# Optimization experiments

Hardware: AMD Instinct MI355X
Metric: run time of the kernel (lower is better)

The kernel has to match this reference:

```python
import jax, jax.numpy as jnp
import numpy as np
import math

B, L, D = 2, 4096, 1024
H, DK, DV = 4, 256, 256
CHUNK = 32
PROB_FLOOR = 0.02


def _l2norm(x, eps=1e-6):
    return x * jax.lax.rsqrt(jnp.sum(x * x, -1, keepdims=True) + eps)


def _silu(x):
    return x * jax.nn.sigmoid(x)


def _short_conv(x, w):
    # x: (b, l, c); w: (c, K). Depthwise causal conv + SiLU (ShortConvolution).
    K = w.shape[-1]
    xp = jnp.pad(x, ((0, 0), (K - 1, 0), (0, 0)))
    y = sum(xp[:, j:j + x.shape[1], :] * w[:, j] for j in range(K))
    return _silu(y)


def _fir_conv(x, filt):
    # x: (b, l, h, d); filt: (h, d, K). Depthwise causal FIR, no activation.
    b, l, h, d = x.shape
    K = filt.shape[-1]
    xf = jnp.pad(x.reshape(b, l, h * d).transpose(0, 2, 1), ((0, 0), (0, 0), (K - 1, 0)))
    w = filt.reshape(h * d, 1, K)
    y = jax.lax.conv_general_dilated(xf, w, (1,), 'VALID',
                                     dimension_numbers=('NCH', 'OIH', 'NCH'),
                                     feature_group_count=h * d)
    return y.transpose(0, 2, 1).reshape(b, l, h, d)


def _delta_rule_chunkwise(q, k, v, beta, chunk=CHUNK):
    # q,k: (b,h,L,dk); v: (b,h,L,dv); beta: (b,h,L). L % chunk == 0.
    b, h, Lq, dk = q.shape
    dv = v.shape[-1]
    n = Lq // chunk
    q = _l2norm(q)
    k = _l2norm(k)
    v = v * beta[..., None]
    kb = k * beta[..., None]
    rs = lambda t: t.reshape(b, h, n, chunk, t.shape[-1])
    qc, kc, vc, kbc = rs(q), rs(k), rs(v), rs(kb)
    strict_lower = jnp.tril(jnp.ones((chunk, chunk), bool), -1)
    # M = strictly-lower part of k_beta @ k^T; the in-place row recursion in the
    # torch code computes (I + M)^{-1} (unit lower-triangular inverse).
    M = jnp.where(strict_lower, jnp.einsum('bhncd,bhnmd->bhncm', kbc, kc), 0.0)
    eye = jnp.eye(chunk, dtype=q.dtype)
    T = jax.scipy.linalg.solve_triangular(eye + M, jnp.broadcast_to(eye, M.shape),
                                          lower=True, unit_diagonal=True)
    u = T @ vc       # (b,h,n,c,dv)
    w = T @ kbc      # (b,h,n,c,dk)
    incl_lower = jnp.tril(jnp.ones((chunk, chunk), bool), 0)

    def step(S, xs):
        q_i, k_i, u_i, w_i = xs  # (b,h,c,d)
        attn = jnp.where(incl_lower, q_i @ k_i.swapaxes(-1, -2), 0.0)
        u_adj = u_i - w_i @ S
        out_i = q_i @ S + attn @ u_adj
        S = S + k_i.swapaxes(-1, -2) @ u_adj
        return S, out_i

    S0 = jnp.zeros((b, h, dk, dv), q.dtype)
    xs = tuple(jnp.moveaxis(t, 2, 0) for t in (qc, kc, u, w))
    S, out = jax.lax.scan(step, S0, xs)
    out = jnp.moveaxis(out, 0, 2).reshape(b, h, Lq, dv)
    return out, S


def _rmsnorm(x, w, eps=1e-5):
    return x * jax.lax.rsqrt(jnp.mean(x * x, -1, keepdims=True) + eps) * w


def _per_head_stats(x):
    mean = jnp.mean(x, -1, keepdims=True)
    var = jnp.var(x, -1, keepdims=True)
    am = jnp.mean(jnp.abs(x), -1, keepdims=True)
    l2 = jnp.sqrt(jnp.sum(x * x, -1, keepdims=True))
    return jnp.concatenate([mean, var, am, l2], -1)  # (...,4)


def setup_inputs() -> dict:
    key = jax.random.key(0)
    ks = jax.random.split(key, 16)
    s = 0.02
    hidden_gate = D * 2 // 2  # fusion_hidden_mult=2 -> 1024
    gate_in_dim = D + 16
    inp = {
        'hidden_states': jax.random.normal(ks[0], (B, L, D), jnp.float32),
        'q_w': jax.random.normal(ks[1], (D, D), jnp.float32) * s,
        'k_w': jax.random.normal(ks[2], (D, D), jnp.float32) * s,
        'v_w': jax.random.normal(ks[3], (D, D), jnp.float32) * s,
        'b_w': jax.random.normal(ks[4], (H, D), jnp.float32) * s,
        'q_cw': jax.random.normal(ks[5], (D, 4), jnp.float32) * s,
        'k_cw': jax.random.normal(ks[6], (D, 4), jnp.float32) * s,
        'v_cw': jax.random.normal(ks[7], (D, 4), jnp.float32) * s,
        'fir_short_w': jax.random.normal(ks[8], (H, DV, 5), jnp.float32) * s,
        'fir_long_w': jax.random.normal(ks[9], (H, DV, 64), jnp.float32) * s,
        'mlp1_w': jax.random.normal(ks[10], (hidden_gate, gate_in_dim), jnp.float32) * s,
        'mlp1_b': jnp.zeros((hidden_gate,), jnp.float32),
        'mlp2_w': jax.random.normal(ks[11], (4, hidden_gate), jnp.float32) * s,
        'mlp2_b': jnp.array([-0.5, -0.5, 1.0, 3.0], jnp.float32),
        'logit_temp': jnp.full((1,), math.log(math.expm1(0.7)), jnp.float32),
        'conv_res_logit': jnp.full((H,), -2.0, jnp.float32),
        'norm_w': jnp.ones((DV,), jnp.float32),
        'o_w': jax.random.normal(ks[12], (D, D), jnp.float32) * s,
    }
    return inp


def _forward(hidden_states, q_w, k_w, v_w, b_w, q_cw, k_cw, v_cw,
             fir_short_w, fir_long_w, mlp1_w, mlp1_b, mlp2_w, mlp2_b,
             logit_temp, conv_res_logit, norm_w, o_w):
    b, l, _ = hidden_states.shape
    # projections + short causal depthwise convs (SiLU, qk_activation='silu')
    q_in = _short_conv(hidden_states @ q_w.T, q_cw)
    k_in = _short_conv(hidden_states @ k_w.T, k_cw)
    v_in = _short_conv(hidden_states @ v_w.T, v_cw)
    q = q_in.reshape(b, l, H, DK)
    k = k_in.reshape(b, l, H, DK)
    v_direct = v_in.reshape(b, l, H, DV)
    # qk_activation='silu' handled in conv; qk_norm='l2' handled inside delta rule
    beta = jnp.maximum(jax.nn.sigmoid(hidden_states @ b_w.T), 1e-6)  # (b,l,H)
    delta_out, _S = _delta_rule_chunkwise(
        q.transpose(0, 2, 1, 3), k.transpose(0, 2, 1, 3),
        v_direct.transpose(0, 2, 1, 3), beta.transpose(0, 2, 1))
    delta_out = delta_out.transpose(0, 2, 1, 3)  # (b,l,H,DV)
    local_short = _fir_conv(v_direct, fir_short_w)
    local_long = _fir_conv(v_direct, fir_long_w)
    stats = jnp.concatenate([_per_head_stats(local_short), _per_head_stats(local_long),
                             _per_head_stats(delta_out), _per_head_stats(v_direct)], -1)  # (b,l,H,16)
    hs_exp = jnp.broadcast_to(hidden_states[:, :, None, :], (b, l, H, hidden_states.shape[-1]))
    gate_in = jnp.concatenate([hs_exp, stats], -1)  # (b,l,H,D+16)
    h1 = jax.nn.gelu(gate_in @ mlp1_w.T + mlp1_b)
    logits = h1 @ mlp2_w.T + mlp2_b  # (b,l,H,4)
    temp = jax.nn.softplus(logit_temp)
    p = jax.nn.softmax(logits / temp, -1)
    p = jnp.maximum(p, PROB_FLOOR)
    p = p / jnp.sum(p, -1, keepdims=True)
    o = (p[..., 0:1] * local_short + p[..., 1:2] * local_long +
         p[..., 2:3] * delta_out + p[..., 3:4] * v_direct)
    # balanced residual conv injection (per-head learned static gate)
    o = o + jax.nn.sigmoid(conv_res_logit)[None, None, :, None] * local_short
    o = _rmsnorm(o, norm_w)
    o = o.reshape(b, l, H * DV) @ o_w.T
    return o


def reference(hidden_states, q_w, k_w, v_w, b_w, q_cw, k_cw, v_cw,
              fir_short_w, fir_long_w, mlp1_w, mlp1_b, mlp2_w, mlp2_b,
              logit_temp, conv_res_logit, norm_w, o_w):
    return _forward(hidden_states, q_w, k_w, v_w, b_w, q_cw, k_cw, v_cw,
                    fir_short_w, fir_long_w, mlp1_w, mlp1_b, mlp2_w, mlp2_b,
                    logit_temp, conv_res_logit, norm_w, o_w)
```

## Files before the change

kernel.cpp:

```cpp
#include <hip/hip_runtime.h>
#include <hip/hip_bf16.h>
#include <math.h>

#define NB 2
#define NL 4096
#define ND 1024
#define NH 4
#define NDK 256
#define NDV 256
#define NCH 128
#define NBL (NB*NL)

typedef __attribute__((ext_vector_type(8))) short short8;
typedef __attribute__((ext_vector_type(4))) short short4v;
typedef __attribute__((ext_vector_type(4))) float float4v;

#define MFMA16(a,b,c) __builtin_amdgcn_mfma_f32_16x16x32_bf16(a,b,c,0,0,0)

__device__ __forceinline__ short f2bs(float f){
  union { __hip_bfloat16 h; short s; } u; u.h = __float2bfloat16(f); return u.s;
}
__device__ __forceinline__ float bs2f(short s){
  union { float f; unsigned u; } u; u.u = ((unsigned)(unsigned short)s) << 16; return u.f;
}
__device__ __forceinline__ void store_c(float* p, float v){ *p = v; }
__device__ __forceinline__ void store_c(short* p, float v){ *p = f2bs(v); }

__device__ __forceinline__ void gload16(const short* g, short* l){
  __builtin_amdgcn_global_load_lds(
      (const __attribute__((address_space(1))) unsigned int*)g,
      (__attribute__((address_space(3))) unsigned int*)l, 16, 0, 0);
}
__device__ __forceinline__ void lds_barrier(){
  asm volatile("s_waitcnt lgkmcnt(0)" ::: "memory");
  __builtin_amdgcn_s_barrier();
  asm volatile("" ::: "memory");
}

__global__ void k_cast8(const float* __restrict__ s, short* __restrict__ d, int n8){
  int i = blockIdx.x*256 + threadIdx.x;
  if(i >= n8) return;
  const float4v a = *(const float4v*)(s + (size_t)i*8);
  const float4v b = *(const float4v*)(s + (size_t)i*8 + 4);
  short8 o;
  #pragma unroll
  for(int j=0;j<4;j++){ o[j] = f2bs(a[j]); o[4+j] = f2bs(b[j]); }
  *(short8*)(d + (size_t)i*8) = o;
}
__global__ void k_cast_w1a(const float* __restrict__ s, short* __restrict__ d){
  int i = blockIdx.x*256 + threadIdx.x;
  int r = i >> 7, c0 = (i & 127)*8;
  const float* sp = s + (size_t)r*1040 + c0;
  const float4v a = *(const float4v*)sp;
  const float4v b = *(const float4v*)(sp + 4);
  short8 o;
  #pragma unroll
  for(int j=0;j<4;j++){ o[j] = f2bs(a[j]); o[4+j] = f2bs(b[j]); }
  *(short8*)(d + (size_t)r*1024 + c0) = o;
}

template<typename OT>
__launch_bounds__(256)
__global__ void k_gemm(const short* __restrict__ A, const short* __restrict__ Bt,
                       OT* __restrict__ C, int M, int N, int K){
  __shared__ short As[128*32];
  __shared__ short Bs[128*32];
  const int tid = threadIdx.x;
  const int w = tid >> 6, lane = tid & 63, lr = lane & 15, lg = lane >> 4;
  const int bm = blockIdx.x*128 + (w >> 1)*64;
  const int bn = blockIdx.y*128 + (w & 1)*64;
  float4v acc[4][4];
  #pragma unroll
  for(int i=0;i<4;i++)
    #pragma unroll
    for(int j=0;j<4;j++) acc[i][j] = (float4v){0.f,0.f,0.f,0.f};
  const short* ga0 = A  + (size_t)(blockIdx.x*128 + (tid>>2))*K + (tid&3)*8;
  const short* ga1 = ga0 + (size_t)64*K;
  const short* gb0 = Bt + (size_t)(blockIdx.y*128 + (tid>>2))*K + (tid&3)*8;
  const short* gb1 = gb0 + (size_t)64*K;
  short* la0 = As + w*512;
  short* la1 = As + 2048 + w*512;
  short* lb0 = Bs + w*512;
  short* lb1 = Bs + 2048 + w*512;
  const int arow = (w>>1)*64, brow = (w&1)*64;
  for(int kk=0; kk<K; kk+=32){
    gload16(ga0+kk, la0);
    gload16(ga1+kk, la1);
    gload16(gb0+kk, lb0);
    gload16(gb1+kk, lb1);
    __syncthreads();
    short8 a[4], b[4];
    #pragma unroll
    for(int i=0;i<4;i++) a[i] = *(const short8*)(As + (arow + i*16 + lr)*32 + lg*8);
    #pragma unroll
    for(int j=0;j<4;j++) b[j] = *(const short8*)(Bs + (brow + j*16 + lr)*32 + lg*8);
    #pragma unroll
    for(int i=0;i<4;i++)
      #pragma unroll
      for(int j=0;j<4;j++)
        acc[i][j] = MFMA16(a[i], b[j], acc[i][j]);
    __syncthreads();
  }
  #pragma unroll
  for(int i=0;i<4;i++){
    int row0 = bm + i*16 + lg*4;
    #pragma unroll
    for(int j=0;j<4;j++){
      OT* cp = C + (size_t)row0*N + bn + j*16 + lr;
      #pragma unroll
      for(int r=0;r<4;r++) store_c(cp + (size_t)r*N, acc[i][j][r]);
    }
  }
}

__global__ void k_conv_silu(const short* __restrict__ x, const float* __restrict__ wgt,
                            short* __restrict__ y){
  int i8 = blockIdx.x*256 + threadIdx.x;
  int c0 = (i8 & 127)*8;
  int l = (i8 >> 7) & (NL-1);
  size_t base = (size_t)i8*8;
  short8 xv[4];
  #pragma unroll
  for(int t=0;t<4;t++)
    xv[t] = (l >= t) ? *(const short8*)(x + base - (size_t)t*1024)
                     : (short8){0,0,0,0,0,0,0,0};
  short8 o;
  #pragma unroll
  for(int j=0;j<8;j++){
    const float4v w4 = *(const float4v*)(wgt + (c0+j)*4);
    float acc = 0.f;
    #pragma unroll
    for(int t=0;t<4;t++) if(l >= t) acc += bs2f(xv[t][j]) * w4[3-t];
    o[j] = f2bs(acc / (1.f + __expf(-acc)));
  }
  *(short8*)(y + base) = o;
}

__global__ void k_beta(const float* __restrict__ hs, const float* __restrict__ bw,
                       float* __restrict__ beta){
  int w = threadIdx.x >> 6, lane = threadIdx.x & 63;
  int bl = blockIdx.x*4 + w;
  const float* x = hs + (size_t)bl*1024;
  float a[4] = {0.f,0.f,0.f,0.f};
  for(int d=lane; d<1024; d+=64){
    float xv = x[d];
    #pragma unroll
    for(int hh=0;hh<4;hh++) a[hh] += xv * bw[hh*1024 + d];
  }
  #pragma unroll
  for(int off=32; off; off>>=1)
    #pragma unroll
    for(int hh=0;hh<4;hh++) a[hh] += __shfl_down(a[hh], off);
  if(lane == 0)
    #pragma unroll
    for(int hh=0;hh<4;hh++)
      beta[(size_t)bl*4 + hh] = fmaxf(1.f/(1.f+__expf(-a[hh])), 1e-6f);
}

#define PADA 260
__launch_bounds__(256)
__global__ void k_phaseA(const short* __restrict__ q, const short* __restrict__ k,
                         const short* __restrict__ v, const float* __restrict__ beta,
                         short* __restrict__ qn_o, short* __restrict__ wn_o,
                         short* __restrict__ kT_o, short* __restrict__ at_o,
                         float* __restrict__ u_o){
  __shared__ float qn[32*PADA];
  __shared__ float kn[32*PADA];
  __shared__ float vb[32*PADA];
  __shared__ float kb[32*PADA];
  __shared__ float Ml[32*33];
  __shared__ float bet[32];
  const int tid = threadIdx.x;
  const int n = blockIdx.x % NCH;
  const int h = (blockIdx.x / NCH) % NH;
  const int b = blockIdx.x / (NCH*NH);
  size_t rowbase = ((size_t)b*NL + n*32)*1024 + h*256;
  if(tid < 32) bet[tid] = beta[((size_t)b*NL + n*32 + tid)*4 + h];
  for(int r=0;r<32;r++){
    qn[r*PADA + tid] = bs2f(q[rowbase + (size_t)r*1024 + tid]);
    kn[r*PADA + tid] = bs2f(k[rowbase + (size_t)r*1024 + tid]);
    vb[r*PADA + tid] = bs2f(v[rowbase + (size_t)r*1024 + tid]);
  }
  __syncthreads();
  {
    int row = tid >> 3, sub = tid & 7;
    float sq = 0.f, sk = 0.f;
    for(int kk=0; kk<32; kk++){
      int d = sub + 8*kk;
      float a0 = qn[row*PADA+d]; sq += a0*a0;
      float a1 = kn[row*PADA+d]; sk += a1*a1;
    }
    #pragma unroll
    for(int off=1; off<8; off<<=1){ sq += __shfl_xor(sq, off); sk += __shfl_xor(sk, off); }
    float rq = rsqrtf(sq + 1e-6f), rk = rsqrtf(sk + 1e-6f);
    float be = bet[row];
    for(int kk=0; kk<32; kk++){
      int d = sub + 8*kk;
      qn[row*PADA+d] *= rq;
      float kv = kn[row*PADA+d]*rk;
      kn[row*PADA+d] = kv;
      kb[row*PADA+d] = kv*be;
      vb[row*PADA+d] *= be;
    }
  }
  __syncthreads();
  {
    int w = tid >> 6, lane = tid & 63, lr = lane & 15, lg = lane >> 4;
    int m0 = (w & 1)*16;
    const float* Asrc = (w < 2) ? kb : qn;
    float4v acc0 = (float4v){0.f,0.f,0.f,0.f}, acc1 = (float4v){0.f,0.f,0.f,0.f};
    for(int kc=0; kc<8; kc++){
      int kof = kc*32 + lg*8;
      short8 af, b0, b1;
      const float* ap  = Asrc + (m0+lr)*PADA + kof;
      const float* bp0 = kn + lr*PADA + kof;
      const float* bp1 = kn + (16+lr)*PADA + kof;
      #pragma unroll
      for(int j=0;j<8;j++){ af[j]=f2bs(ap[j]); b0[j]=f2bs(bp0[j]); b1[j]=f2bs(bp1[j]); }
      acc0 = MFMA16(af, b0, acc0);
      acc1 = MFMA16(af, b1, acc1);
    }
    if(w < 2){
      #pragma unroll
      for(int r=0;r<4;r++){
        int row = m0 + lg*4 + r;
        Ml[row*33 + lr]      = (lr      < row) ? acc0[r] : 0.f;
        Ml[row*33 + 16 + lr] = ((16+lr) < row) ? acc1[r] : 0.f;
      }
    } else {
      size_t abase = (size_t)blockIdx.x * 1024;
      #pragma unroll
      for(int r=0;r<4;r++){
        int row = m0 + lg*4 + r;
        at_o[abase + row*32 + lr]      = (lr      <= row) ? f2bs(acc0[r]) : (short)0;
        at_o[abase + row*32 + 16 + lr] = ((16+lr) <= row) ? f2bs(acc1[r]) : (short)0;
      }
    }
  }
  __syncthreads();
  {
    int d = tid;
    for(int i=1;i<32;i++){
      float su = 0.f, sw = 0.f;
      const float* Mr = Ml + i*33;
      for(int t=0;t<i;t++){
        float m = Mr[t];
        su += m * vb[t*PADA + d];
        sw += m * kb[t*PADA + d];
      }
      vb[i*PADA + d] -= su;
      kb[i*PADA + d] -= sw;
    }
  }
  __syncthreads();
  {
    size_t obase = (size_t)blockIdx.x * 8192;
    for(int it=0; it<32; it++){
      int idx = it*256 + tid;
      qn_o[obase + idx] = f2bs(qn[it*PADA + tid]);
      wn_o[obase + idx] = f2bs(-kb[it*PADA + tid]);
      u_o [obase + idx] = vb[it*PADA + tid];
      int tt = idx & 31, dd = idx >> 5;
      kT_o[obase + idx] = f2bs(kn[tt*PADA + dd]);
    }
  }
}

struct FragsB {
  short8 a[8];
  short8 kt[4];
  short8 at;
  float4v u;
};

__device__ __forceinline__ void loadFrags(FragsB& f, size_t cb,
    const short* __restrict__ qn, const short* __restrict__ wn,
    const short* __restrict__ kT, const short* __restrict__ at,
    const float* __restrict__ u, int w, int lr, int lg, int m0, int c0){
  const short* kT_b = kT + cb*8192;
  #pragma unroll
  for(int mi=0;mi<4;mi++)
    f.kt[mi] = *(const short8*)(kT_b + ((w*4+mi)*16 + lr)*32 + lg*8);
  if(w < 2){
    const short* wn_b = wn + cb*8192;
    #pragma unroll
    for(int kc=0;kc<8;kc++)
      f.a[kc] = *(const short8*)(wn_b + (m0+lr)*256 + kc*32 + lg*8);
    const float* up = u + cb*8192 + (size_t)(m0 + lg*4)*256 + c0 + lr;
    #pragma unroll
    for(int r=0;r<4;r++) f.u[r] = up[(size_t)r*256];
  } else {
    const short* qn_b = qn + cb*8192;
    #pragma unroll
    for(int kc=0;kc<8;kc++)
      f.a[kc] = *(const short8*)(qn_b + (m0+lr)*256 + kc*32 + lg*8);
    f.at = *(const short8*)(at + cb*1024 + (m0+lr)*32 + lg*8);
  }
}

__device__ __forceinline__ void computeChunk(const FragsB& f, int n,
    float4v (&Sreg)[4], float* __restrict__ ua, short* __restrict__ ScT,
    short* __restrict__ dout, int b, int h, int c0,
    int w, int lr, int lg, int m0, int swz){
  char* scb = (char*)ScT;
  lds_barrier();
  float4v oacc = (float4v){0.f,0.f,0.f,0.f};
  if(w < 2){
    float4v acc = f.u, acc2 = (float4v){0.f,0.f,0.f,0.f};
    #pragma unroll
    for(int kc=0;kc<4;kc++){
      short8 s0 = *(const short8*)(scb + (((lr<<9) + ((kc*32 + lg*8)<<1)) ^ swz));
      short8 s1 = *(const short8*)(scb + (((lr<<9) + (((kc+4)*32 + lg*8)<<1)) ^ swz));
      acc  = MFMA16(f.a[kc],   s0, acc);
      acc2 = MFMA16(f.a[kc+4], s1, acc2);
    }
    #pragma unroll
    for(int r=0;r<4;r++) ua[(m0 + lg*4 + r)*18 + lr] = acc[r] + acc2[r];
  } else {
    float4v acc2 = (float4v){0.f,0.f,0.f,0.f};
    #pragma unroll
    for(int kc=0;kc<4;kc++){
      short8 s0 = *(const short8*)(scb + (((lr<<9) + ((kc*32 + lg*8)<<1)) ^ swz));
      short8 s1 = *(const short8*)(scb + (((lr<<9) + (((kc+4)*32 + lg*8)<<1)) ^ swz));
      oacc = MFMA16(f.a[kc],   s0, oacc);
      acc2 = MFMA16(f.a[kc+4], s1, acc2);
    }
    #pragma unroll
    for(int r=0;r<4;r++) oacc[r] += acc2[r];
  }
  lds_barrier();
  short8 bu;
  #pragma unroll
  for(int j=0;j<8;j++) bu[j] = f2bs(ua[(lg*8 + j)*18 + lr]);
  if(w >= 2){
    oacc = MFMA16(f.at, bu, oacc);
    short* ob = dout + ((size_t)b*NL + n*32 + m0 + lg*4)*1024 + h*256 + c0 + lr;
    #pragma unroll
    for(int r=0;r<4;r++) ob[(size_t)r*1024] = f2bs(oacc[r]);
  }
  #pragma unroll
  for(int mi=0; mi<4; mi++){
    Sreg[mi] = MFMA16(f.kt[mi], bu, Sreg[mi]);
    int rowb = (w*4 + mi)*16 + lg*4;
    short4v pk;
    #pragma unroll
    for(int r=0;r<4;r++) pk[r] = f2bs(Sreg[mi][r]);
    *(short4v*)(scb + (((lr<<9) + (rowb<<1)) ^ swz)) = pk;
  }
}

__launch_bounds__(256, 1)
__global__ void k_phaseB(const short* __restrict__ qn, const short* __restrict__ wn,
                         const short* __restrict__ kT, const short* __restrict__ at,
                         const float* __restrict__ u, short* __restrict__ dout){
  __shared__ float ua[32*18];
  __shared__ short ScT[4096];
  const int tid = threadIdx.x;
  const int chain = blockIdx.x & 7;
  const int cblk = blockIdx.x >> 3;
  const int b = chain >> 2, h = chain & 3;
  const int c0 = cblk * 16;
  for(int i=tid; i<4096; i+=256) ScT[i] = 0;
  const int w = tid >> 6, lane = tid & 63, lr = lane & 15, lg = lane >> 4;
  const int m0 = (w & 1)*16;
  const size_t chunkbase = (size_t)(b*NH + h) * NCH;
  const int swz = (lr & 7) << 4;
  float4v Sreg[4];
  #pragma unroll
  for(int mi=0;mi<4;mi++) Sreg[mi] = (float4v){0.f,0.f,0.f,0.f};
  __syncthreads();
  FragsB fA, fB;
  loadFrags(fA, chunkbase, qn, wn, kT, at, u, w, lr, lg, m0, c0);
  for(int n=0; n<NCH; n+=2){
    loadFrags(fB, chunkbase + n+1, qn, wn, kT, at, u, w, lr, lg, m0, c0);
    computeChunk(fA, n, Sreg, ua, ScT, dout, b, h, c0, w, lr, lg, m0, swz);
    if(n+2 < NCH)
      loadFrags(fA, chunkbase + n+2, qn, wn, kT, at, u, w, lr, lg, m0, c0);
    computeChunk(fB, n+1, Sreg, ua, ScT, dout, b, h, c0, w, lr, lg, m0, swz);
  }
}

__launch_bounds__(256, 2)
__global__ void k_fir(const short* __restrict__ v, const float* __restrict__ wS,
                      const float* __restrict__ wL, short* __restrict__ ls,
                      short* __restrict__ ll){
  const int tid = threadIdx.x;
  const int lt = blockIdx.x % (NL/32);
  const int h = (blockIdx.x / (NL/32)) % NH;
  const int b = blockIdx.x / ((NL/32)*NH);
  const int l0 = lt*32;
  const size_t colbase = (size_t)b*NL*1024 + h*256 + tid;
  const float* wLp = wL + (size_t)h*16384 + tid*64;
  const float* wSp = wS + (size_t)h*1280 + tid*5;
  float accL[32], accS[32];
  #pragma unroll
  for(int i=0;i<32;i++){ accL[i]=0.f; accS[i]=0.f; }
  {
    float w[32];
    #pragma unroll
    for(int j=0;j<32;j++) w[j] = wLp[j];
    float val[63];
    #pragma unroll
    for(int s=0;s<63;s++){
      int l = l0 - 63 + s;
      int lc = l < 0 ? 0 : l;
      float x = bs2f(v[colbase + (size_t)lc*1024]);
      val[s] = l < 0 ? 0.f : x;
    }
    #pragma unroll
    for(int i=0;i<32;i++)
      #pragma unroll
      for(int j=0;j<32;j++)
        accL[i] += val[i+j]*w[j];
  }
  {
    float w[32];
    #pragma unroll
    for(int j=0;j<32;j++) w[j] = wLp[32+j];
    float w5[5];
    #pragma unroll
    for(int j=0;j<5;j++) w5[j] = wSp[j];
    float val[63];
    #pragma unroll
    for(int s=0;s<63;s++){
      int l = l0 - 31 + s;
      int lc = l < 0 ? 0 : l;
      float x = bs2f(v[colbase + (size_t)lc*1024]);
      val[s] = l < 0 ? 0.f : x;
    }
    #pragma unroll
    for(int i=0;i<32;i++){
      #pragma unroll
      for(int j=0;j<32;j++)
        accL[i] += val[i+j]*w[j];
      #pragma unroll
      for(int j=0;j<5;j++)
        accS[i] += val[i+27+j]*w5[j];
    }
  }
  #pragma unroll
  for(int i=0;i<32;i++){
    size_t ox = colbase + (size_t)(l0+i)*1024;
    ll[ox] = f2bs(accL[i]);
    ls[ox] = f2bs(accS[i]);
  }
}

__launch_bounds__(256)
__global__ void k_gate(const short* __restrict__ ls, const short* __restrict__ ll,
                       const short* __restrict__ dd, const short* __restrict__ vv,
                       const short* __restrict__ G, const float* __restrict__ w1,
                       const float* __restrict__ b1, const float* __restrict__ w2,
                       const float* __restrict__ b2, const float* __restrict__ ltp,
                       float* __restrict__ p){
  __shared__ float st[4][16];
  __shared__ float red[4][4];
  const int tid = threadIdx.x;
  const size_t bl = blockIdx.x;
  {
    int row = tid >> 4, ln = tid & 15;
    int ten = row >> 2, hh = row & 3;
    const short* base = (ten==0 ? ls : ten==1 ? ll : ten==2 ? dd : vv) + (bl*4 + hh)*256;
    float s1=0.f, s2=0.f, sa=0.f;
    for(int kk=0; kk<16; kk++){
      float x = bs2f(base[ln + 16*kk]);
      s1 += x; s2 += x*x; sa += fabsf(x);
    }
    #pragma unroll
    for(int off=1; off<16; off<<=1){
      s1 += __shfl_xor(s1, off); s2 += __shfl_xor(s2, off); sa += __shfl_xor(sa, off);
    }
    if(ln == 0){
      float mean = s1 * (1.f/256.f);
      st[hh][ten*4+0] = mean;
      st[hh][ten*4+1] = s2*(1.f/256.f) - mean*mean;
      st[hh][ten*4+2] = sa*(1.f/256.f);
      st[hh][ten*4+3] = sqrtf(s2);
    }
  }
  __syncthreads();
  const int w = tid >> 6, lane = tid & 63;
  float temp = log1pf(__expf(ltp[0]));
  for(int hh=0; hh<4; hh++){
    float sreg[16];
    #pragma unroll
    for(int s=0;s<16;s++) sreg[s] = st[hh][s];
    float lg4[4] = {0.f,0.f,0.f,0.f};
    for(int ii=0; ii<4; ii++){
      int i = tid + ii*256;
      float g = bs2f(G[bl*1024 + i]) + b1[i];
      const float* wr = w1 + (size_t)i*1040 + 1024;
      #pragma unroll
      for(int s=0;s<16;s++) g += sreg[s]*wr[s];
      float z = 1.5957691216057308f*(g + 0.044715f*g*g*g);
      float hg = g / (1.f + __expf(-z));
      #pragma unroll
      for(int jj=0;jj<4;jj++) lg4[jj] += hg * w2[jj*1024 + i];
    }
    #pragma unroll
    for(int off=32; off; off>>=1)
      #pragma unroll
      for(int jj=0;jj<4;jj++) lg4[jj] += __shfl_down(lg4[jj], off);
    if(lane == 0)
      #pragma unroll
      for(int jj=0;jj<4;jj++) red[w][jj] = lg4[jj];
    __syncthreads();
    if(tid == 0){
      float lo[4]; float mx = -1e30f;
      #pragma unroll
      for(int jj=0;jj<4;jj++){
        lo[jj] = (red[0][jj]+red[1][jj]+red[2][jj]+red[3][jj] + b2[jj]) / temp;
        mx = fmaxf(mx, lo[jj]);
      }
      float e[4], se = 0.f;
      #pragma unroll
      for(int jj=0;jj<4;jj++){ e[jj] = __expf(lo[jj]-mx); se += e[jj]; }
      float s2 = 0.f;
      #pragma unroll
      for(int jj=0;jj<4;jj++){ e[jj] = fmaxf(e[jj]/se, 0.02f); s2 += e[jj]; }
      float inv = 1.f/s2;
      #pragma unroll
      for(int jj=0;jj<4;jj++) p[bl*16 + hh*4 + jj] = e[jj]*inv;
    }
    __syncthreads();
  }
}

__launch_bounds__(256)
__global__ void k_combine(const float* __restrict__ p, const short* __restrict__ ls,
                          const short* __restrict__ ll, const short* __restrict__ dd,
                          const short* __restrict__ vv, const float* __restrict__ crl,
                          const float* __restrict__ nw, short* __restrict__ obf){
  __shared__ float red[4];
  const size_t bl = blockIdx.x >> 2;
  const int h = blockIdx.x & 3;
  const int tid = threadIdx.x;
  size_t ix = bl*1024 + h*256 + tid;
  const float* pp = p + bl*16 + h*4;
  float rg = 1.f/(1.f + __expf(-crl[h]));
  float o = (pp[0] + rg)*bs2f(ls[ix]) + pp[1]*bs2f(ll[ix]) + pp[2]*bs2f(dd[ix]) + pp[3]*bs2f(vv[ix]);
  float ss = o*o;
  int w = tid >> 6, lane = tid & 63;
  #pragma unroll
  for(int off=32; off; off>>=1) ss += __shfl_down(ss, off);
  if(lane == 0) red[w] = ss;
  __syncthreads();
  float tot = red[0]+red[1]+red[2]+red[3];
  float rms = rsqrtf(tot*(1.f/256.f) + 1e-5f);
  obf[ix] = f2bs(o*rms*nw[tid]);
}

extern "C" void kernel_launch(void* const* d_in, const int* in_sizes, int n_in,
                              void* d_out, int out_size, void* d_ws, size_t ws_size,
                              hipStream_t stream){
  const float* hs  = (const float*)d_in[0];
  const float* qw  = (const float*)d_in[1];
  const float* kw  = (const float*)d_in[2];
  const float* vw  = (const float*)d_in[3];
  const float* bw  = (const float*)d_in[4];
  const float* qcw = (const float*)d_in[5];
  const float* kcw = (const float*)d_in[6];
  const float* vcw = (const float*)d_in[7];
  const float* fsw = (const float*)d_in[8];
  const float* flw = (const float*)d_in[9];
  const float* w1  = (const float*)d_in[10];
  const float* b1  = (const float*)d_in[11];
  const float* w2  = (const float*)d_in[12];
  const float* b2  = (const float*)d_in[13];
  const float* ltp = (const float*)d_in[14];
  const float* crl = (const float*)d_in[15];
  const float* nw  = (const float*)d_in[16];
  const float* ow  = (const float*)d_in[17];

  char* ws = (char*)d_ws;
  size_t off = 0;
  auto alloc = [&](size_t bytes)->char*{
    char* pp = ws + off; off += (bytes + 255) & ~(size_t)255; return pp;
  };
  short* hs_bf  = (short*)alloc((size_t)NBL*1024*2);
  short* wbuf   = (short*)alloc((size_t)1024*1024*2);
  short* qp_bf  = (short*)alloc((size_t)NBL*1024*2);
  short* kp_bf  = (short*)alloc((size_t)NBL*1024*2);
  short* vp_bf  = (short*)alloc((size_t)NBL*1024*2);
  short* qc_bf  = (short*)alloc((size_t)NBL*1024*2);
  short* kc_bf  = (short*)alloc((size_t)NBL*1024*2);
  short* vc_bf  = (short*)alloc((size_t)NBL*1024*2);
  float* u_f    = (float*)alloc((size_t)NBL*1024*4);
  short* do_bf  = (short*)alloc((size_t)NBL*1024*2);
  short* at_bf  = (short*)alloc((size_t)NB*NH*NCH*1024*2);
  float* beta   = (float*)alloc((size_t)NBL*4*4);
  float* pbuf   = (float*)alloc((size_t)NBL*16*4);
  if(ws_size < off) return;

  short* qn_bf = qp_bf; short* wn_bf = kp_bf; short* kT_bf = vp_bf;
  short* ls_bf = qc_bf; short* ll_bf = kc_bf;
  short* G_bf  = vp_bf;
  short* o_bf  = kp_bf;

  dim3 gg(64, 8);
  k_cast8<<<dim3(4096),dim3(256),0,stream>>>(hs, hs_bf, NBL*1024/8);
  k_cast8<<<dim3(512),dim3(256),0,stream>>>(qw, wbuf, 1024*1024/8);
  k_gemm<short><<<gg,dim3(256),0,stream>>>(hs_bf, wbuf, qp_bf, NBL, 1024, 1024);
  k_cast8<<<dim3(512),dim3(256),0,stream>>>(kw, wbuf, 1024*1024/8);
  k_gemm<short><<<gg,dim3(256),0,stream>>>(hs_bf, wbuf, kp_bf, NBL, 1024, 1024);
  k_cast8<<<dim3(512),dim3(256),0,stream>>>(vw, wbuf, 1024*1024/8);
  k_gemm<short><<<gg,dim3(256),0,stream>>>(hs_bf, wbuf, vp_bf, NBL, 1024, 1024);
  k_conv_silu<<<dim3(4096),dim3(256),0,stream>>>(qp_bf, qcw, qc_bf);
  k_conv_silu<<<dim3(4096),dim3(256),0,stream>>>(kp_bf, kcw, kc_bf);
  k_conv_silu<<<dim3(4096),dim3(256),0,stream>>>(vp_bf, vcw, vc_bf);
  k_beta<<<dim3(2048),dim3(256),0,stream>>>(hs, bw, beta);
  k_phaseA<<<dim3(1024),dim3(256),0,stream>>>(qc_bf, kc_bf, vc_bf, beta,
                                              qn_bf, wn_bf, kT_bf, at_bf, u_f);
  k_phaseB<<<dim3(128),dim3(256),0,stream>>>(qn_bf, wn_bf, kT_bf, at_bf, u_f, do_bf);
  k_fir<<<dim3(1024),dim3(256),0,stream>>>(vc_bf, fsw, flw, ls_bf, ll_bf);
  k_cast_w1a<<<dim3(512),dim3(256),0,stream>>>(w1, wbuf);
  k_gemm<short><<<gg,dim3(256),0,stream>>>(hs_bf, wbuf, G_bf, NBL, 1024, 1024);
  k_gate<<<dim3(8192),dim3(256),0,stream>>>(ls_bf, ll_bf, do_bf, vc_bf, G_bf,
                                            w1, b1, w2, b2, ltp, pbuf);
  k_combine<<<dim3(32768),dim3(256),0,stream>>>(pbuf, ls_bf, ll_bf, do_bf, vc_bf,
                                                crl, nw, o_bf);
  k_cast8<<<dim3(512),dim3(256),0,stream>>>(ow, wbuf, 1024*1024/8);
  k_gemm<float><<<gg,dim3(256),0,stream>>>(o_bf, wbuf, (float*)d_out, NBL, 1024, 1024);
}
```

Measured before the change: 636.1 us.

## Batch QKV and gate projections into one GEMM and fuse gate with combine

Concatenates the q, k, v and gate-MLP first-layer weights into one bf16 buffer and runs a single 2048-block GEMM that routes output column tiles to four separate destinations. This replaces four serial GEMM launches and lets all four run concurrently on the GPU. The gate kernel is also merged with the combine/RMSNorm kernel, so the mixing probabilities stay in shared memory and the combine reads happen in the same block. The cost is a larger workspace and a dedicated G buffer instead of reusing vp_bf.

```diff
diff --git a/kernel.cpp b/kernel.cpp
--- a/kernel.cpp
+++ b/kernel.cpp
@@ -57,6 +57,63 @@
   #pragma unroll
   for(int j=0;j<4;j++){ o[j] = f2bs(a[j]); o[4+j] = f2bs(b[j]); }
   *(short8*)(d + (size_t)r*1024 + c0) = o;
+}
+
+__launch_bounds__(256)
+__global__ void k_gemm4(const short* __restrict__ A, const short* __restrict__ Bt,
+                        short* __restrict__ oq, short* __restrict__ ok,
+                        short* __restrict__ ov, short* __restrict__ og){
+  const int K = 1024;
+  __shared__ short As[128*32];
+  __shared__ short Bs[128*32];
+  const int tid = threadIdx.x;
+  const int w = tid >> 6, lane = tid & 63, lr = lane & 15, lg = lane >> 4;
+  const int bm = blockIdx.x*128 + (w >> 1)*64;
+  const int bnl = (blockIdx.y & 7)*128 + (w & 1)*64;
+  short* C = (blockIdx.y>>3)==0 ? oq : (blockIdx.y>>3)==1 ? ok
+           : (blockIdx.y>>3)==2 ? ov : og;
+  float4v acc[4][4];
+  #pragma unroll
+  for(int i=0;i<4;i++)
+    #pragma unroll
+    for(int j=0;j<4;j++) acc[i][j] = (float4v){0.f,0.f,0.f,0.f};
+  const short* ga0 = A  + (size_t)(blockIdx.x*128 + (tid>>2))*K + (tid&3)*8;
+  const short* ga1 = ga0 + (size_t)64*K;
+  const short* gb0 = Bt + (size_t)(blockIdx.y*128 + (tid>>2))*K + (tid&3)*8;
+  const short* gb1 = gb0 + (size_t)64*K;
+  short* la0 = As + w*512;
+  short* la1 = As + 2048 + w*512;
+  short* lb0 = Bs + w*512;
+  short* lb1 = Bs + 2048 + w*512;
+  const int arow = (w>>1)*64, brow = (w&1)*64;
+  for(int kk=0; kk<K; kk+=32){
+    gload16(ga0+kk, la0);
+    gload16(ga1+kk, la1);
+    gload16(gb0+kk, lb0);
+    gload16(gb1+kk, lb1);
+    __syncthreads();
+    short8 a[4], b[4];
+    #pragma unroll
+    for(int i=0;i<4;i++) a[i] = *(const short8*)(As + (arow + i*16 + lr)*32 + lg*8);
+    #pragma unroll
+    for(int j=0;j<4;j++) b[j] = *(const short8*)(Bs + (brow + j*16 + lr)*32 + lg*8);
+    #pragma unroll
+    for(int i=0;i<4;i++)
+      #pragma unroll
+      for(int j=0;j<4;j++)
+        acc[i][j] = MFMA16(a[i], b[j], acc[i][j]);
+    __syncthreads();
+  }
+  #pragma unroll
+  for(int i=0;i<4;i++){
+    int row0 = bm + i*16 + lg*4;
+    #pragma unroll
+    for(int j=0;j<4;j++){
+      short* cp = C + (size_t)row0*1024 + bnl + j*16 + lr;
+      #pragma unroll
+      for(int r=0;r<4;r++) cp[(size_t)r*1024] = f2bs(acc[i][j][r]);
+    }
+  }
 }
 
 template<typename OT>
@@ -447,14 +504,17 @@
 }
 
 __launch_bounds__(256)
-__global__ void k_gate(const short* __restrict__ ls, const short* __restrict__ ll,
-                       const short* __restrict__ dd, const short* __restrict__ vv,
-                       const short* __restrict__ G, const float* __restrict__ w1,
-                       const float* __restrict__ b1, const float* __restrict__ w2,
-                       const float* __restrict__ b2, const float* __restrict__ ltp,
-                       float* __restrict__ p){
+__global__ void k_gatecomb(const short* __restrict__ ls, const short* __restrict__ ll,
+                           const short* __restrict__ dd, const short* __restrict__ vv,
+                           const short* __restrict__ G, const float* __restrict__ w1,
+                           const float* __restrict__ b1, const float* __restrict__ w2,
+                           const float* __restrict__ b2, const float* __restrict__ ltp,
+                           const float* __restrict__ crl, const float* __restrict__ nw,
+                           short* __restrict__ obf){
   __shared__ float st[4][16];
   __shared__ float red[4][4];
+  __shared__ float pl[4][4];
+  __shared__ float rr2[4][4];
   const int tid = threadIdx.x;
   const size_t bl = blockIdx.x;
   {
@@ -520,34 +580,36 @@
       for(int jj=0;jj<4;jj++){ e[jj] = fmaxf(e[jj]/se, 0.02f); s2 += e[jj]; }
       float inv = 1.f/s2;
       #pragma unroll
-      for(int jj=0;jj<4;jj++) p[bl*16 + hh*4 + jj] = e[jj]*inv;
+      for(int jj=0;jj<4;jj++) pl[hh][jj] = e[jj]*inv;
     }
     __syncthreads();
   }
-}
-
-__launch_bounds__(256)
-__global__ void k_combine(const float* __restrict__ p, const short* __restrict__ ls,
-                          const short* __restrict__ ll, const short* __restrict__ dd,
-                          const short* __restrict__ vv, const float* __restrict__ crl,
-                          const float* __restrict__ nw, short* __restrict__ obf){
-  __shared__ float red[4];
-  const size_t bl = blockIdx.x >> 2;
-  const int h = blockIdx.x & 3;
-  const int tid = threadIdx.x;
-  size_t ix = bl*1024 + h*256 + tid;
-  const float* pp = p + bl*16 + h*4;
-  float rg = 1.f/(1.f + __expf(-crl[h]));
-  float o = (pp[0] + rg)*bs2f(ls[ix]) + pp[1]*bs2f(ll[ix]) + pp[2]*bs2f(dd[ix]) + pp[3]*bs2f(vv[ix]);
-  float ss = o*o;
-  int w = tid >> 6, lane = tid & 63;
-  #pragma unroll
-  for(int off=32; off; off>>=1) ss += __shfl_down(ss, off);
-  if(lane == 0) red[w] = ss;
+  float o4[4], ss4[4];
+  #pragma unroll
+  for(int h=0; h<4; h++){
+    size_t ix = (bl*4 + h)*256 + tid;
+    float rg = 1.f/(1.f + __expf(-crl[h]));
+    float o = (pl[h][0] + rg)*bs2f(ls[ix]) + pl[h][1]*bs2f(ll[ix])
+            + pl[h][2]*bs2f(dd[ix]) + pl[h][3]*bs2f(vv[ix]);
+    o4[h] = o;
+    ss4[h] = o*o;
+  }
+  #pragma unroll
+  for(int off=32; off; off>>=1)
+    #pragma unroll
+    for(int h=0; h<4; h++) ss4[h] += __shfl_down(ss4[h], off);
+  if(lane == 0)
+    #pragma unroll
+    for(int h=0; h<4; h++) rr2[w][h] = ss4[h];
   __syncthreads();
-  float tot = red[0]+red[1]+red[2]+red[3];
-  float rms = rsqrtf(tot*(1.f/256.f) + 1e-5f);
-  obf[ix] = f2bs(o*rms*nw[tid]);
+  float nwv = nw[tid];
+  #pragma unroll
+  for(int h=0; h<4; h++){
+    float tot = rr2[0][h]+rr2[1][h]+rr2[2][h]+rr2[3][h];
+    float rms = rsqrtf(tot*(1.f/256.f) + 1e-5f);
+    size_t ix = (bl*4 + h)*256 + tid;
+    obf[ix] = f2bs(o4[h]*rms*nwv);
+  }
 }
 
 extern "C" void kernel_launch(void* const* d_in, const int* in_sizes, int n_in,
@@ -578,10 +640,11 @@
     char* pp = ws + off; off += (bytes + 255) & ~(size_t)255; return pp;
   };
   short* hs_bf  = (short*)alloc((size_t)NBL*1024*2);
-  short* wbuf   = (short*)alloc((size_t)1024*1024*2);
+  short* wmega  = (short*)alloc((size_t)4096*1024*2);
   short* qp_bf  = (short*)alloc((size_t)NBL*1024*2);
   short* kp_bf  = (short*)alloc((size_t)NBL*1024*2);
   short* vp_bf  = (short*)alloc((size_t)NBL*1024*2);
+  short* g_bf   = (short*)alloc((size_t)NBL*1024*2);
   short* qc_bf  = (short*)alloc((size_t)NBL*1024*2);
   short* kc_bf  = (short*)alloc((size_t)NBL*1024*2);
   short* vc_bf  = (short*)alloc((size_t)NBL*1024*2);
@@ -589,22 +652,18 @@
   short* do_bf  = (short*)alloc((size_t)NBL*1024*2);
   short* at_bf  = (short*)alloc((size_t)NB*NH*NCH*1024*2);
   float* beta   = (float*)alloc((size_t)NBL*4*4);
-  float* pbuf   = (float*)alloc((size_t)NBL*16*4);
   if(ws_size < off) return;
 
   short* qn_bf = qp_bf; short* wn_bf = kp_bf; short* kT_bf = vp_bf;
   short* ls_bf = qc_bf; short* ll_bf = kc_bf;
-  short* G_bf  = vp_bf;
   short* o_bf  = kp_bf;
 
-  dim3 gg(64, 8);
   k_cast8<<<dim3(4096),dim3(256),0,stream>>>(hs, hs_bf, NBL*1024/8);
-  k_cast8<<<dim3(512),dim3(256),0,stream>>>(qw, wbuf, 1024*1024/8);
-  k_gemm<short><<<gg,dim3(256),0,stream>>>(hs_bf, wbuf, qp_bf, NBL, 1024, 1024);
-  k_cast8<<<dim3(512),dim3(256),0,stream>>>(kw, wbuf, 1024*1024/8);
-  k_gemm<short><<<gg,dim3(256),0,stream>>>(hs_bf, wbuf, kp_bf, NBL, 1024, 1024);
-  k_cast8<<<dim3(512),dim3(256),0,stream>>>(vw, wbuf, 1024*1024/8);
-  k_gemm<short><<<gg,dim3(256),0,stream>>>(hs_bf, wbuf, vp_bf, NBL, 1024, 1024);
+  k_cast8<<<dim3(512),dim3(256),0,stream>>>(qw, wmega, 1024*1024/8);
+  k_cast8<<<dim3(512),dim3(256),0,stream>>>(kw, wmega + 1024*1024, 1024*1024/8);
+  k_cast8<<<dim3(512),dim3(256),0,stream>>>(vw, wmega + 2*1024*1024, 1024*1024/8);
+  k_cast_w1a<<<dim3(512),dim3(256),0,stream>>>(w1, wmega + 3*1024*1024);
+  k_gemm4<<<dim3(64,32),dim3(256),0,stream>>>(hs_bf, wmega, qp_bf, kp_bf, vp_bf, g_bf);
   k_conv_silu<<<dim3(4096),dim3(256),0,stream>>>(qp_bf, qcw, qc_bf);
   k_conv_silu<<<dim3(4096),dim3(256),0,stream>>>(kp_bf, kcw, kc_bf);
   k_conv_silu<<<dim3(4096),dim3(256),0,stream>>>(vp_bf, vcw, vc_bf);
@@ -613,12 +672,9 @@
                                               qn_bf, wn_bf, kT_bf, at_bf, u_f);
   k_phaseB<<<dim3(128),dim3(256),0,stream>>>(qn_bf, wn_bf, kT_bf, at_bf, u_f, do_bf);
   k_fir<<<dim3(1024),dim3(256),0,stream>>>(vc_bf, fsw, flw, ls_bf, ll_bf);
-  k_cast_w1a<<<dim3(512),dim3(256),0,stream>>>(w1, wbuf);
-  k_gemm<short><<<gg,dim3(256),0,stream>>>(hs_bf, wbuf, G_bf, NBL, 1024, 1024);
-  k_gate<<<dim3(8192),dim3(256),0,stream>>>(ls_bf, ll_bf, do_bf, vc_bf, G_bf,
-                                            w1, b1, w2, b2, ltp, pbuf);
-  k_combine<<<dim3(32768),dim3(256),0,stream>>>(pbuf, ls_bf, ll_bf, do_bf, vc_bf,
-                                                crl, nw, o_bf);
-  k_cast8<<<dim3(512),dim3(256),0,stream>>>(ow, wbuf, 1024*1024/8);
-  k_gemm<float><<<gg,dim3(256),0,stream>>>(o_bf, wbuf, (float*)d_out, NBL, 1024, 1024);
-}
+  k_gatecomb<<<dim3(8192),dim3(256),0,stream>>>(ls_bf, ll_bf, do_bf, vc_bf, g_bf,
+                                                w1, b1, w2, b2, ltp, crl, nw, o_bf);
+  k_cast8<<<dim3(512),dim3(256),0,stream>>>(ow, wmega, 1024*1024/8);
+  k_gemm<float><<<dim3(64,8),dim3(256),0,stream>>>(o_bf, wmega, (float*)d_out,
+                                                   NBL, 1024, 1024);
+}
```

After: 587.6 us. 7.6% less time.
